# Optimization experiments

Hardware: AMD Instinct MI355X
Metric: run time of the kernel (lower is better)

Reference implementation:

```python
import jax, jax.numpy as jnp
import numpy as np

IN_DIM, OUT_DIM = 64, 64
HIDDEN = [64, 64, 64]
D = IN_DIM * OUT_DIM  # number of independent per-edge small MLPs
B = 256


def setup_inputs() -> dict:
    key = jax.random.key(0)
    ks = jax.random.split(key, 10)

    def kaiming(k, shape, fan_in):
        # kaiming_uniform_ with a=0, nonlinearity='relu': bound = sqrt(6/fan_in)
        bound = np.sqrt(6.0 / fan_in)
        return jax.random.uniform(k, shape, jnp.float32, -bound, bound)

    def bias_init(k, shape, fan_in):
        bound = 1.0 / np.sqrt(fan_in)
        return jax.random.uniform(k, shape, jnp.float32, -bound, bound)

    h0, h1, h2 = HIDDEN
    inp = {
        "x": jax.random.normal(ks[0], (B, IN_DIM), jnp.float32),
        # Input_Linear: weight (out_dim, in_dim, h0); fan_in per torch kaiming on this tensor is in_dim*h0,
        # bias uses reset_parameters(1) -> fan_in=1
        "w0": kaiming(ks[1], (OUT_DIM, IN_DIM, h0), IN_DIM * h0),
        "b0": bias_init(ks[2], (D, h0), 1),
        # Linear(d, o=h1, i=h0): weight (d, h1, h0); kaiming fan_in = h0 (last dim), bias fan_in = i = h0
        "w1": kaiming(ks[3], (D, h1, h0), h0),
        "b1": bias_init(ks[4], (D, h1), h0),
        "w2": kaiming(ks[5], (D, h2, h1), h1),
        "b2": bias_init(ks[6], (D, h2), h1),
        # Output_Linear: weight (out_dim, in_dim*h2), fan_in = in_dim*h2
        "wout": kaiming(ks[7], (OUT_DIM, IN_DIM * h2), IN_DIM * h2),
        "bout": bias_init(ks[8], (OUT_DIM,), IN_DIM * h2),
    }
    return inp


def reference(x, w0, b0, w1, b1, w2, b2, wout, bout):
    Bsz = x.shape[0]
    # Input_Linear: broadcast outer product -> (B, out_dim, in_dim, h0) -> (B, d, h0)
    out = x[:, None, :, None] * w0[None, :, :, :]
    out = out.reshape(Bsz, D, HIDDEN[0]) + b0[None, :, :]
    out = jax.nn.relu(out)
    # Hidden per-edge Linear layers: 'doi,Bdi->Bdo'
    out = jnp.einsum('doi,bdi->bdo', w1, out) + b1[None, :, :]
    out = jax.nn.relu(out)
    out = jnp.einsum('doi,bdi->bdo', w2, out) + b2[None, :, :]
    out = jax.nn.relu(out)
    # Output_Linear: (B, d, h2) -> (B, out_dim, in_dim*h2); 'oi,boi->bo'
    xv = out.reshape(Bsz, OUT_DIM, IN_DIM * HIDDEN[-1])
    return jnp.einsum('oi,boi->bo', wout, xv) + bout[None, :]
```

## Files before the change

### kernel.cpp

```cpp
#include <hip/hip_runtime.h>
#include <hip/hip_bf16.h>


#define D_EDGES 4096

typedef __attribute__((ext_vector_type(4))) float f32x4;
typedef __attribute__((ext_vector_type(8))) short bf16x8;

__device__ __forceinline__ unsigned pk2(float a, float b) {
    __hip_bfloat162 h = __float22bfloat162_rn(float2{a, b});
    return *reinterpret_cast<unsigned*>(&h);
}

union BFr { unsigned u[4]; bf16x8 v; };

__global__ __launch_bounds__(256, 3) void kan_mfma(
    const float* __restrict__ x,
    const float* __restrict__ w0g,
    const float* __restrict__ b0g,
    const float* __restrict__ w1g,
    const float* __restrict__ b1g,
    const float* __restrict__ w2g,
    const float* __restrict__ b2g,
    const float* __restrict__ woutg,
    float* __restrict__ outbuf,
    int atomic_mode)
{
    const int d = blockIdx.x, o = d >> 6, ii = d & 63;
    const int t = threadIdx.x;
    const int lane = t & 63, wv = t >> 6;

    __shared__ __align__(16) unsigned char W1s[64 * 128];
    __shared__ __align__(16) unsigned char W2s[64 * 128];
    __shared__ __align__(16) unsigned char Hs[256 * 128];
    __shared__ __align__(16) float sx[256];
    __shared__ __align__(16) float sw0[64], sb0[64], sb1[64], sb2[64], swo[64];

    {
        const int orow = t >> 2, q = t & 3;
        const unsigned swz  = (unsigned)((orow & 7) << 4);
        const unsigned base = (unsigned)(orow * 128);
        const float* s1 = w1g + (size_t)d * 4096 + orow * 64 + q * 16;
        const float* s2 = w2g + (size_t)d * 4096 + orow * 64 + q * 16;

        float4 a0 = ((const float4*)s1)[0], a1 = ((const float4*)s1)[1];
        float4 a2 = ((const float4*)s1)[2], a3 = ((const float4*)s1)[3];
        uint4 u0 = { pk2(a0.x, a0.y), pk2(a0.z, a0.w), pk2(a1.x, a1.y), pk2(a1.z, a1.w) };
        uint4 u1 = { pk2(a2.x, a2.y), pk2(a2.z, a2.w), pk2(a3.x, a3.y), pk2(a3.z, a3.w) };
        *(uint4*)&W1s[base + ((unsigned)(q * 32)      ^ swz)] = u0;
        *(uint4*)&W1s[base + ((unsigned)(q * 32 + 16) ^ swz)] = u1;

        a0 = ((const float4*)s2)[0]; a1 = ((const float4*)s2)[1];
        a2 = ((const float4*)s2)[2]; a3 = ((const float4*)s2)[3];
        uint4 v0 = { pk2(a0.x, a0.y), pk2(a0.z, a0.w), pk2(a1.x, a1.y), pk2(a1.z, a1.w) };
        uint4 v1 = { pk2(a2.x, a2.y), pk2(a2.z, a2.w), pk2(a3.x, a3.y), pk2(a3.z, a3.w) };
        *(uint4*)&W2s[base + ((unsigned)(q * 32)      ^ swz)] = v0;
        *(uint4*)&W2s[base + ((unsigned)(q * 32 + 16) ^ swz)] = v1;
    }
    sx[t] = x[t * 64 + ii];
    if (t < 64) {
        sw0[t] = w0g[(size_t)d * 64 + t];
        sb0[t] = b0g[(size_t)d * 64 + t];
        sb1[t] = b1g[(size_t)d * 64 + t];
        sb2[t] = b2g[(size_t)d * 64 + t];
        swo[t] = woutg[(size_t)o * 4096 + ii * 64 + t];
    }
    __syncthreads();

    const int arow = lane & 15;
    const int kb   = (lane >> 4) * 16;
    const int g8   = (lane >> 4) * 8;
    const unsigned lswz = (unsigned)((lane & 7) << 4);
    const int mbase = wv * 64;
    const int r0 = (lane >> 4) * 4;
    const f32x4 zero4 = { 0.f, 0.f, 0.f, 0.f };

    bf16x8 wf1[4][2];
#pragma unroll
    for (int nt = 0; nt < 4; ++nt)
#pragma unroll
        for (int ks = 0; ks < 2; ++ks)
            wf1[nt][ks] = *(const bf16x8*)&W1s[(nt * 16 + arow) * 128 +
                            ((unsigned)(ks * 64 + kb) ^ lswz)];

    float4 w0v[2][2], b0v[2][2];
#pragma unroll
    for (int ks = 0; ks < 2; ++ks) {
        const int k0 = ks * 32 + g8;
        w0v[ks][0] = *(const float4*)&sw0[k0];
        w0v[ks][1] = *(const float4*)&sw0[k0 + 4];
        b0v[ks][0] = *(const float4*)&sb0[k0];
        b0v[ks][1] = *(const float4*)&sb0[k0 + 4];
    }

    f32x4 acc[4][4];
#pragma unroll
    for (int i = 0; i < 4; ++i)
#pragma unroll
        for (int j = 0; j < 4; ++j) acc[i][j] = zero4;

#pragma unroll
    for (int mti = 0; mti < 4; ++mti) {
        const float xm = sx[mbase + mti * 16 + arow];
#pragma unroll
        for (int ks = 0; ks < 2; ++ks) {
            float4 wa = w0v[ks][0], wb = w0v[ks][1];
            float4 ba = b0v[ks][0], bb = b0v[ks][1];
            float v0 = fmaxf(fmaf(xm, wa.x, ba.x), 0.f);
            float v1 = fmaxf(fmaf(xm, wa.y, ba.y), 0.f);
            float v2 = fmaxf(fmaf(xm, wa.z, ba.z), 0.f);
            float v3 = fmaxf(fmaf(xm, wa.w, ba.w), 0.f);
            float v4 = fmaxf(fmaf(xm, wb.x, bb.x), 0.f);
            float v5 = fmaxf(fmaf(xm, wb.y, bb.y), 0.f);
            float v6 = fmaxf(fmaf(xm, wb.z, bb.z), 0.f);
            float v7 = fmaxf(fmaf(xm, wb.w, bb.w), 0.f);
            BFr bh;
            bh.u[0] = pk2(v0, v1); bh.u[1] = pk2(v2, v3);
            bh.u[2] = pk2(v4, v5); bh.u[3] = pk2(v6, v7);
#pragma unroll
            for (int nt = 0; nt < 4; ++nt)
                acc[mti][nt] = __builtin_amdgcn_mfma_f32_16x16x32_bf16(
                    wf1[nt][ks], bh.v, acc[mti][nt], 0, 0, 0);
        }
    }

#pragma unroll
    for (int mti = 0; mti < 4; ++mti) {
        const unsigned rb = (unsigned)((mbase + mti * 16 + arow) * 128);
#pragma unroll
        for (int nt = 0; nt < 4; ++nt) {
            float4 bv = *(const float4*)&sb1[nt * 16 + r0];
            float v0 = fmaxf(acc[mti][nt][0] + bv.x, 0.f);
            float v1 = fmaxf(acc[mti][nt][1] + bv.y, 0.f);
            float v2 = fmaxf(acc[mti][nt][2] + bv.z, 0.f);
            float v3 = fmaxf(acc[mti][nt][3] + bv.w, 0.f);
            uint2 hp = { pk2(v0, v1), pk2(v2, v3) };
            *(uint2*)&Hs[rb + ((unsigned)(2 * (nt * 16 + r0)) ^ lswz)] = hp;
        }
    }

    asm volatile("s_waitcnt lgkmcnt(0)" ::: "memory");

    bf16x8 wf2[4][2];
#pragma unroll
    for (int nt = 0; nt < 4; ++nt)
#pragma unroll
        for (int ks = 0; ks < 2; ++ks)
            wf2[nt][ks] = *(const bf16x8*)&W2s[(nt * 16 + arow) * 128 +
                            ((unsigned)(ks * 64 + kb) ^ lswz)];

#pragma unroll
    for (int i = 0; i < 4; ++i)
#pragma unroll
        for (int j = 0; j < 4; ++j) acc[i][j] = zero4;

#pragma unroll
    for (int mti = 0; mti < 4; ++mti) {
        const unsigned rb = (unsigned)((mbase + mti * 16 + arow) * 128);
#pragma unroll
        for (int ks = 0; ks < 2; ++ks) {
            bf16x8 bh = *(const bf16x8*)&Hs[rb + ((unsigned)(ks * 64 + kb) ^ lswz)];
#pragma unroll
            for (int nt = 0; nt < 4; ++nt)
                acc[mti][nt] = __builtin_amdgcn_mfma_f32_16x16x32_bf16(
                    wf2[nt][ks], bh, acc[mti][nt], 0, 0, 0);
        }
    }

#pragma unroll
    for (int mti = 0; mti < 4; ++mti) {
        float p = 0.f;
#pragma unroll
        for (int nt = 0; nt < 4; ++nt) {
            float4 bv = *(const float4*)&sb2[nt * 16 + r0];
            float4 wo = *(const float4*)&swo[nt * 16 + r0];
            p = fmaf(fmaxf(acc[mti][nt][0] + bv.x, 0.f), wo.x, p);
            p = fmaf(fmaxf(acc[mti][nt][1] + bv.y, 0.f), wo.y, p);
            p = fmaf(fmaxf(acc[mti][nt][2] + bv.z, 0.f), wo.z, p);
            p = fmaf(fmaxf(acc[mti][nt][3] + bv.w, 0.f), wo.w, p);
        }
        p += __shfl_xor(p, 16);
        p += __shfl_xor(p, 32);
        const int b = mbase + mti * 16 + arow;
        if (lane < 16) {
            if (atomic_mode) atomicAdd(&outbuf[b * 64 + o], p);
            else             outbuf[(size_t)d * 256 + b] = p;
        }
    }
}

__global__ __launch_bounds__(256) void kan_reduce(
    const float* __restrict__ partial,
    const float* __restrict__ bout,
    float* __restrict__ y)
{
    const int o = blockIdx.x;
    const int b = threadIdx.x;
    float acc = bout[o];
    const float* p = partial + (size_t)o * (64 * 256) + b;
#pragma unroll
    for (int i = 0; i < 64; ++i)
        acc += p[i * 256];
    y[b * 64 + o] = acc;
}

__global__ __launch_bounds__(256) void kan_init_out(const float* __restrict__ bout,
                                                    float* __restrict__ y)
{
    const int idx = blockIdx.x * 256 + threadIdx.x;
    y[idx] = bout[idx & 63];
}

extern "C" void kernel_launch(void* const* d_in, const int* in_sizes, int n_in,
                              void* d_out, int out_size, void* d_ws, size_t ws_size,
                              hipStream_t stream) {
    const float* x    = (const float*)d_in[0];
    const float* w0   = (const float*)d_in[1];
    const float* b0   = (const float*)d_in[2];
    const float* w1   = (const float*)d_in[3];
    const float* b1   = (const float*)d_in[4];
    const float* w2   = (const float*)d_in[5];
    const float* b2   = (const float*)d_in[6];
    const float* wout = (const float*)d_in[7];
    const float* bout = (const float*)d_in[8];
    float* y = (float*)d_out;

    const size_t partial_bytes = (size_t)D_EDGES * 256 * sizeof(float);

    if (ws_size >= partial_bytes) {
        float* partial = (float*)d_ws;
        kan_mfma<<<D_EDGES, 256, 0, stream>>>(x, w0, b0, w1, b1, w2, b2, wout, partial, 0);
        kan_reduce<<<64, 256, 0, stream>>>(partial, bout, y);
    } else {
        kan_init_out<<<64, 256, 0, stream>>>(bout, y);
        kan_mfma<<<D_EDGES, 256, 0, stream>>>(x, w0, b0, w1, b1, w2, b2, wout, y, 1);
    }
}
```

Baseline: 43.25 us.

## Process four edges per block with register-prefetched weights and per-tile hidden staging

New measurement: 105.8 us. 2.45x slower.

```diff
diff --git a/kernel.cpp b/kernel.cpp
--- a/kernel.cpp
+++ b/kernel.cpp
@@ -3,6 +3,7 @@
 
 
 #define D_EDGES 4096
+#define EPB 4
 
 typedef __attribute__((ext_vector_type(4))) float f32x4;
 typedef __attribute__((ext_vector_type(8))) short bf16x8;
@@ -26,165 +27,169 @@
     float* __restrict__ outbuf,
     int atomic_mode)
 {
-    const int d = blockIdx.x, o = d >> 6, ii = d & 63;
     const int t = threadIdx.x;
     const int lane = t & 63, wv = t >> 6;
+    const int d0 = blockIdx.x * EPB;
 
     __shared__ __align__(16) unsigned char W1s[64 * 128];
     __shared__ __align__(16) unsigned char W2s[64 * 128];
-    __shared__ __align__(16) unsigned char Hs[256 * 128];
+    __shared__ __align__(16) unsigned char Hs[4 * 16 * 128];
     __shared__ __align__(16) float sx[256];
     __shared__ __align__(16) float sw0[64], sb0[64], sb1[64], sb2[64], swo[64];
 
-    {
-        const int orow = t >> 2, q = t & 3;
-        const unsigned swz  = (unsigned)((orow & 7) << 4);
-        const unsigned base = (unsigned)(orow * 128);
-        const float* s1 = w1g + (size_t)d * 4096 + orow * 64 + q * 16;
-        const float* s2 = w2g + (size_t)d * 4096 + orow * 64 + q * 16;
-
-        float4 a0 = ((const float4*)s1)[0], a1 = ((const float4*)s1)[1];
-        float4 a2 = ((const float4*)s1)[2], a3 = ((const float4*)s1)[3];
-        uint4 u0 = { pk2(a0.x, a0.y), pk2(a0.z, a0.w), pk2(a1.x, a1.y), pk2(a1.z, a1.w) };
-        uint4 u1 = { pk2(a2.x, a2.y), pk2(a2.z, a2.w), pk2(a3.x, a3.y), pk2(a3.z, a3.w) };
-        *(uint4*)&W1s[base + ((unsigned)(q * 32)      ^ swz)] = u0;
-        *(uint4*)&W1s[base + ((unsigned)(q * 32 + 16) ^ swz)] = u1;
-
-        a0 = ((const float4*)s2)[0]; a1 = ((const float4*)s2)[1];
-        a2 = ((const float4*)s2)[2]; a3 = ((const float4*)s2)[3];
-        uint4 v0 = { pk2(a0.x, a0.y), pk2(a0.z, a0.w), pk2(a1.x, a1.y), pk2(a1.z, a1.w) };
-        uint4 v1 = { pk2(a2.x, a2.y), pk2(a2.z, a2.w), pk2(a3.x, a3.y), pk2(a3.z, a3.w) };
-        *(uint4*)&W2s[base + ((unsigned)(q * 32)      ^ swz)] = v0;
-        *(uint4*)&W2s[base + ((unsigned)(q * 32 + 16) ^ swz)] = v1;
-    }
-    sx[t] = x[t * 64 + ii];
-    if (t < 64) {
-        sw0[t] = w0g[(size_t)d * 64 + t];
-        sb0[t] = b0g[(size_t)d * 64 + t];
-        sb1[t] = b1g[(size_t)d * 64 + t];
-        sb2[t] = b2g[(size_t)d * 64 + t];
-        swo[t] = woutg[(size_t)o * 4096 + ii * 64 + t];
-    }
+    const int orow = t >> 2, q = t & 3;
+    const unsigned wswz  = (unsigned)((orow & 7) << 4);
+    const unsigned wbase = (unsigned)(orow * 128);
+
+    float4 s1r[4], s2r[4];
+    float xv = 0.f, w0r = 0.f, b0r = 0.f, b1r = 0.f, b2r = 0.f, wor = 0.f;
+
+    auto load_edge = [&](int dd) {
+        const float* s1 = w1g + (size_t)dd * 4096 + orow * 64 + q * 16;
+        const float* s2 = w2g + (size_t)dd * 4096 + orow * 64 + q * 16;
+        s1r[0] = ((const float4*)s1)[0]; s1r[1] = ((const float4*)s1)[1];
+        s1r[2] = ((const float4*)s1)[2]; s1r[3] = ((const float4*)s1)[3];
+        s2r[0] = ((const float4*)s2)[0]; s2r[1] = ((const float4*)s2)[1];
+        s2r[2] = ((const float4*)s2)[2]; s2r[3] = ((const float4*)s2)[3];
+        xv = x[t * 64 + (dd & 63)];
+        if (t < 64) {
+            w0r = w0g[(size_t)dd * 64 + t];
+            b0r = b0g[(size_t)dd * 64 + t];
+            b1r = b1g[(size_t)dd * 64 + t];
+            b2r = b2g[(size_t)dd * 64 + t];
+            wor = woutg[(size_t)(dd >> 6) * 4096 + (dd & 63) * 64 + t];
+        }
+    };
+
+    auto store_edge = [&]() {
+        uint4 u0 = { pk2(s1r[0].x, s1r[0].y), pk2(s1r[0].z, s1r[0].w),
+                     pk2(s1r[1].x, s1r[1].y), pk2(s1r[1].z, s1r[1].w) };
+        uint4 u1 = { pk2(s1r[2].x, s1r[2].y), pk2(s1r[2].z, s1r[2].w),
+                     pk2(s1r[3].x, s1r[3].y), pk2(s1r[3].z, s1r[3].w) };
+        *(uint4*)&W1s[wbase + ((unsigned)(q * 32)      ^ wswz)] = u0;
+        *(uint4*)&W1s[wbase + ((unsigned)(q * 32 + 16) ^ wswz)] = u1;
+        uint4 v0 = { pk2(s2r[0].x, s2r[0].y), pk2(s2r[0].z, s2r[0].w),
+                     pk2(s2r[1].x, s2r[1].y), pk2(s2r[1].z, s2r[1].w) };
+        uint4 v1 = { pk2(s2r[2].x, s2r[2].y), pk2(s2r[2].z, s2r[2].w),
+                     pk2(s2r[3].x, s2r[3].y), pk2(s2r[3].z, s2r[3].w) };
+        *(uint4*)&W2s[wbase + ((unsigned)(q * 32)      ^ wswz)] = v0;
+        *(uint4*)&W2s[wbase + ((unsigned)(q * 32 + 16) ^ wswz)] = v1;
+        sx[t] = xv;
+        if (t < 64) {
+            sw0[t] = w0r; sb0[t] = b0r; sb1[t] = b1r; sb2[t] = b2r; swo[t] = wor;
+        }
+    };
+
+    load_edge(d0);
+    store_edge();
     __syncthreads();
 
     const int arow = lane & 15;
     const int kb   = (lane >> 4) * 16;
     const int g8   = (lane >> 4) * 8;
     const unsigned lswz = (unsigned)((lane & 7) << 4);
-    const int mbase = wv * 64;
     const int r0 = (lane >> 4) * 4;
+    const unsigned hbase = (unsigned)(wv * 2048 + arow * 128);
+    const unsigned hswz  = (unsigned)((arow & 7) << 4);
     const f32x4 zero4 = { 0.f, 0.f, 0.f, 0.f };
 
-    bf16x8 wf1[4][2];
-#pragma unroll
-    for (int nt = 0; nt < 4; ++nt)
-#pragma unroll
-        for (int ks = 0; ks < 2; ++ks)
-            wf1[nt][ks] = *(const bf16x8*)&W1s[(nt * 16 + arow) * 128 +
-                            ((unsigned)(ks * 64 + kb) ^ lswz)];
-
-    float4 w0v[2][2], b0v[2][2];
-#pragma unroll
-    for (int ks = 0; ks < 2; ++ks) {
-        const int k0 = ks * 32 + g8;
-        w0v[ks][0] = *(const float4*)&sw0[k0];
-        w0v[ks][1] = *(const float4*)&sw0[k0 + 4];
-        b0v[ks][0] = *(const float4*)&sb0[k0];
-        b0v[ks][1] = *(const float4*)&sb0[k0 + 4];
-    }
-
-    f32x4 acc[4][4];
-#pragma unroll
-    for (int i = 0; i < 4; ++i)
-#pragma unroll
-        for (int j = 0; j < 4; ++j) acc[i][j] = zero4;
-
-#pragma unroll
-    for (int mti = 0; mti < 4; ++mti) {
-        const float xm = sx[mbase + mti * 16 + arow];
+    for (int e = 0; e < EPB; ++e) {
+        const int d = d0 + e;
+        const int o = d >> 6;
+
+        if (e + 1 < EPB) load_edge(d + 1);
+
+        bf16x8 wf1[4][2], wf2[4][2];
+#pragma unroll
+        for (int nt = 0; nt < 4; ++nt)
+#pragma unroll
+            for (int ks = 0; ks < 2; ++ks) {
+                wf1[nt][ks] = *(const bf16x8*)&W1s[(nt * 16 + arow) * 128 +
+                                ((unsigned)(ks * 64 + kb) ^ lswz)];
+                wf2[nt][ks] = *(const bf16x8*)&W2s[(nt * 16 + arow) * 128 +
+                                ((unsigned)(ks * 64 + kb) ^ lswz)];
+            }
+
+        float4 w0v[2][2], b0v[2][2];
 #pragma unroll
         for (int ks = 0; ks < 2; ++ks) {
-            float4 wa = w0v[ks][0], wb = w0v[ks][1];
-            float4 ba = b0v[ks][0], bb = b0v[ks][1];
-            float v0 = fmaxf(fmaf(xm, wa.x, ba.x), 0.f);
-            float v1 = fmaxf(fmaf(xm, wa.y, ba.y), 0.f);
-            float v2 = fmaxf(fmaf(xm, wa.z, ba.z), 0.f);
-            float v3 = fmaxf(fmaf(xm, wa.w, ba.w), 0.f);
-            float v4 = fmaxf(fmaf(xm, wb.x, bb.x), 0.f);
-            float v5 = fmaxf(fmaf(xm, wb.y, bb.y), 0.f);
-            float v6 = fmaxf(fmaf(xm, wb.z, bb.z), 0.f);
-            float v7 = fmaxf(fmaf(xm, wb.w, bb.w), 0.f);
-            BFr bh;
-            bh.u[0] = pk2(v0, v1); bh.u[1] = pk2(v2, v3);
-            bh.u[2] = pk2(v4, v5); bh.u[3] = pk2(v6, v7);
-#pragma unroll
-            for (int nt = 0; nt < 4; ++nt)
-                acc[mti][nt] = __builtin_amdgcn_mfma_f32_16x16x32_bf16(
-                    wf1[nt][ks], bh.v, acc[mti][nt], 0, 0, 0);
-        }
-    }
-
-#pragma unroll
-    for (int mti = 0; mti < 4; ++mti) {
-        const unsigned rb = (unsigned)((mbase + mti * 16 + arow) * 128);
-#pragma unroll
-        for (int nt = 0; nt < 4; ++nt) {
-            float4 bv = *(const float4*)&sb1[nt * 16 + r0];
-            float v0 = fmaxf(acc[mti][nt][0] + bv.x, 0.f);
-            float v1 = fmaxf(acc[mti][nt][1] + bv.y, 0.f);
-            float v2 = fmaxf(acc[mti][nt][2] + bv.z, 0.f);
-            float v3 = fmaxf(acc[mti][nt][3] + bv.w, 0.f);
-            uint2 hp = { pk2(v0, v1), pk2(v2, v3) };
-            *(uint2*)&Hs[rb + ((unsigned)(2 * (nt * 16 + r0)) ^ lswz)] = hp;
-        }
-    }
-
-    asm volatile("s_waitcnt lgkmcnt(0)" ::: "memory");
-
-    bf16x8 wf2[4][2];
-#pragma unroll
-    for (int nt = 0; nt < 4; ++nt)
-#pragma unroll
-        for (int ks = 0; ks < 2; ++ks)
-            wf2[nt][ks] = *(const bf16x8*)&W2s[(nt * 16 + arow) * 128 +
-                            ((unsigned)(ks * 64 + kb) ^ lswz)];
-
-#pragma unroll
-    for (int i = 0; i < 4; ++i)
-#pragma unroll
-        for (int j = 0; j < 4; ++j) acc[i][j] = zero4;
-
-#pragma unroll
-    for (int mti = 0; mti < 4; ++mti) {
-        const unsigned rb = (unsigned)((mbase + mti * 16 + arow) * 128);
-#pragma unroll
-        for (int ks = 0; ks < 2; ++ks) {
-            bf16x8 bh = *(const bf16x8*)&Hs[rb + ((unsigned)(ks * 64 + kb) ^ lswz)];
-#pragma unroll
-            for (int nt = 0; nt < 4; ++nt)
-                acc[mti][nt] = __builtin_amdgcn_mfma_f32_16x16x32_bf16(
-                    wf2[nt][ks], bh, acc[mti][nt], 0, 0, 0);
-        }
-    }
-
-#pragma unroll
-    for (int mti = 0; mti < 4; ++mti) {
-        float p = 0.f;
-#pragma unroll
-        for (int nt = 0; nt < 4; ++nt) {
-            float4 bv = *(const float4*)&sb2[nt * 16 + r0];
-            float4 wo = *(const float4*)&swo[nt * 16 + r0];
-            p = fmaf(fmaxf(acc[mti][nt][0] + bv.x, 0.f), wo.x, p);
-            p = fmaf(fmaxf(acc[mti][nt][1] + bv.y, 0.f), wo.y, p);
-            p = fmaf(fmaxf(acc[mti][nt][2] + bv.z, 0.f), wo.z, p);
-            p = fmaf(fmaxf(acc[mti][nt][3] + bv.w, 0.f), wo.w, p);
-        }
-        p += __shfl_xor(p, 16);
-        p += __shfl_xor(p, 32);
-        const int b = mbase + mti * 16 + arow;
-        if (lane < 16) {
-            if (atomic_mode) atomicAdd(&outbuf[b * 64 + o], p);
-            else             outbuf[(size_t)d * 256 + b] = p;
+            const int k0 = ks * 32 + g8;
+            w0v[ks][0] = *(const float4*)&sw0[k0];
+            w0v[ks][1] = *(const float4*)&sw0[k0 + 4];
+            b0v[ks][0] = *(const float4*)&sb0[k0];
+            b0v[ks][1] = *(const float4*)&sb0[k0 + 4];
+        }
+
+#pragma unroll
+        for (int mti = 0; mti < 4; ++mti) {
+            const float xm = sx[wv * 64 + mti * 16 + arow];
+
+            f32x4 a1[4] = { zero4, zero4, zero4, zero4 };
+#pragma unroll
+            for (int ks = 0; ks < 2; ++ks) {
+                float4 wa = w0v[ks][0], wb = w0v[ks][1];
+                float4 ba = b0v[ks][0], bb = b0v[ks][1];
+                float v0 = fmaxf(fmaf(xm, wa.x, ba.x), 0.f);
+                float v1 = fmaxf(fmaf(xm, wa.y, ba.y), 0.f);
+                float v2 = fmaxf(fmaf(xm, wa.z, ba.z), 0.f);
+                float v3 = fmaxf(fmaf(xm, wa.w, ba.w), 0.f);
+                float v4 = fmaxf(fmaf(xm, wb.x, bb.x), 0.f);
+                float v5 = fmaxf(fmaf(xm, wb.y, bb.y), 0.f);
+                float v6 = fmaxf(fmaf(xm, wb.z, bb.z), 0.f);
+                float v7 = fmaxf(fmaf(xm, wb.w, bb.w), 0.f);
+                BFr bh;
+                bh.u[0] = pk2(v0, v1); bh.u[1] = pk2(v2, v3);
+                bh.u[2] = pk2(v4, v5); bh.u[3] = pk2(v6, v7);
+#pragma unroll
+                for (int nt = 0; nt < 4; ++nt)
+                    a1[nt] = __builtin_amdgcn_mfma_f32_16x16x32_bf16(
+                        wf1[nt][ks], bh.v, a1[nt], 0, 0, 0);
+            }
+
+#pragma unroll
+            for (int nt = 0; nt < 4; ++nt) {
+                float4 bv = *(const float4*)&sb1[nt * 16 + r0];
+                float v0 = fmaxf(a1[nt][0] + bv.x, 0.f);
+                float v1 = fmaxf(a1[nt][1] + bv.y, 0.f);
+                float v2 = fmaxf(a1[nt][2] + bv.z, 0.f);
+                float v3 = fmaxf(a1[nt][3] + bv.w, 0.f);
+                uint2 hp = { pk2(v0, v1), pk2(v2, v3) };
+                *(uint2*)&Hs[hbase + ((unsigned)(2 * (nt * 16 + r0)) ^ hswz)] = hp;
+            }
+
+            f32x4 a2[4] = { zero4, zero4, zero4, zero4 };
+#pragma unroll
+            for (int ks = 0; ks < 2; ++ks) {
+                bf16x8 bh2 = *(const bf16x8*)&Hs[hbase + ((unsigned)(ks * 64 + kb) ^ hswz)];
+#pragma unroll
+                for (int nt = 0; nt < 4; ++nt)
+                    a2[nt] = __builtin_amdgcn_mfma_f32_16x16x32_bf16(
+                        wf2[nt][ks], bh2, a2[nt], 0, 0, 0);
+            }
+
+            float p = 0.f;
+#pragma unroll
+            for (int nt = 0; nt < 4; ++nt) {
+                float4 bv = *(const float4*)&sb2[nt * 16 + r0];
+                float4 wo = *(const float4*)&swo[nt * 16 + r0];
+                p = fmaf(fmaxf(a2[nt][0] + bv.x, 0.f), wo.x, p);
+                p = fmaf(fmaxf(a2[nt][1] + bv.y, 0.f), wo.y, p);
+                p = fmaf(fmaxf(a2[nt][2] + bv.z, 0.f), wo.z, p);
+                p = fmaf(fmaxf(a2[nt][3] + bv.w, 0.f), wo.w, p);
+            }
+            p += __shfl_xor(p, 16);
+            p += __shfl_xor(p, 32);
+            const int b = wv * 64 + mti * 16 + arow;
+            if (lane < 16) {
+                if (atomic_mode) atomicAdd(&outbuf[b * 64 + o], p);
+                else             outbuf[(size_t)d * 256 + b] = p;
+            }
+        }
+
+        if (e + 1 < EPB) {
+            __syncthreads();
+            store_edge();
+            __syncthreads();
         }
     }
 }
@@ -226,13 +231,14 @@
     float* y = (float*)d_out;
 
     const size_t partial_bytes = (size_t)D_EDGES * 256 * sizeof(float);
+    const int nblk = D_EDGES / EPB;
 
     if (ws_size >= partial_bytes) {
         float* partial = (float*)d_ws;
-        kan_mfma<<<D_EDGES, 256, 0, stream>>>(x, w0, b0, w1, b1, w2, b2, wout, partial, 0);
+        kan_mfma<<<nblk, 256, 0, stream>>>(x, w0, b0, w1, b1, w2, b2, wout, partial, 0);
         kan_reduce<<<64, 256, 0, stream>>>(partial, bout, y);
     } else {
         kan_init_out<<<64, 256, 0, stream>>>(bout, y);
-        kan_mfma<<<D_EDGES, 256, 0, stream>>>(x, w0, b0, w1, b1, w2, b2, wout, y, 1);
+        kan_mfma<<<nblk, 256, 0, stream>>>(x, w0, b0, w1, b1, w2, b2, wout, y, 1);
     }
 }
```

## Fuse both hidden layers per 16-row tile to shrink LDS and registers

Applied to the files above, without the earlier changes.

Result: no change. 42.67 us (-1.4%).

```diff
diff --git a/kernel.cpp b/kernel.cpp
--- a/kernel.cpp
+++ b/kernel.cpp
@@ -14,7 +14,7 @@
 
 union BFr { unsigned u[4]; bf16x8 v; };
 
-__global__ __launch_bounds__(256, 3) void kan_mfma(
+__global__ __launch_bounds__(256, 4) void kan_mfma(
     const float* __restrict__ x,
     const float* __restrict__ w0g,
     const float* __restrict__ b0g,
@@ -32,7 +32,7 @@
 
     __shared__ __align__(16) unsigned char W1s[64 * 128];
     __shared__ __align__(16) unsigned char W2s[64 * 128];
-    __shared__ __align__(16) unsigned char Hs[256 * 128];
+    __shared__ __align__(16) unsigned char Hs[4 * 16 * 128];
     __shared__ __align__(16) float sx[256];
     __shared__ __align__(16) float sw0[64], sb0[64], sb1[64], sb2[64], swo[64];
 
@@ -71,8 +71,9 @@
     const int kb   = (lane >> 4) * 16;
     const int g8   = (lane >> 4) * 8;
     const unsigned lswz = (unsigned)((lane & 7) << 4);
-    const int mbase = wv * 64;
     const int r0 = (lane >> 4) * 4;
+    const unsigned hbase = (unsigned)(wv * 2048 + arow * 128);
+    const unsigned hswz  = (unsigned)((arow & 7) << 4);
     const f32x4 zero4 = { 0.f, 0.f, 0.f, 0.f };
 
     bf16x8 wf1[4][2];
@@ -93,15 +94,11 @@
         b0v[ks][1] = *(const float4*)&sb0[k0 + 4];
     }
 
-    f32x4 acc[4][4];
-#pragma unroll
-    for (int i = 0; i < 4; ++i)
-#pragma unroll
-        for (int j = 0; j < 4; ++j) acc[i][j] = zero4;
-
 #pragma unroll
     for (int mti = 0; mti < 4; ++mti) {
-        const float xm = sx[mbase + mti * 16 + arow];
+        const float xm = sx[wv * 64 + mti * 16 + arow];
+
+        f32x4 a1[4] = { zero4, zero4, zero4, zero4 };
 #pragma unroll
         for (int ks = 0; ks < 2; ++ks) {
             float4 wa = w0v[ks][0], wb = w0v[ks][1];
@@ -119,69 +116,47 @@
             bh.u[2] = pk2(v4, v5); bh.u[3] = pk2(v6, v7);
 #pragma unroll
             for (int nt = 0; nt < 4; ++nt)
-                acc[mti][nt] = __builtin_amdgcn_mfma_f32_16x16x32_bf16(
-                    wf1[nt][ks], bh.v, acc[mti][nt], 0, 0, 0);
-        }
-    }
-
-#pragma unroll
-    for (int mti = 0; mti < 4; ++mti) {
-        const unsigned rb = (unsigned)((mbase + mti * 16 + arow) * 128);
+                a1[nt] = __builtin_amdgcn_mfma_f32_16x16x32_bf16(
+                    wf1[nt][ks], bh.v, a1[nt], 0, 0, 0);
+        }
+
 #pragma unroll
         for (int nt = 0; nt < 4; ++nt) {
             float4 bv = *(const float4*)&sb1[nt * 16 + r0];
-            float v0 = fmaxf(acc[mti][nt][0] + bv.x, 0.f);
-            float v1 = fmaxf(acc[mti][nt][1] + bv.y, 0.f);
-            float v2 = fmaxf(acc[mti][nt][2] + bv.z, 0.f);
-            float v3 = fmaxf(acc[mti][nt][3] + bv.w, 0.f);
+            float v0 = fmaxf(a1[nt][0] + bv.x, 0.f);
+            float v1 = fmaxf(a1[nt][1] + bv.y, 0.f);
+            float v2 = fmaxf(a1[nt][2] + bv.z, 0.f);
+            float v3 = fmaxf(a1[nt][3] + bv.w, 0.f);
             uint2 hp = { pk2(v0, v1), pk2(v2, v3) };
-            *(uint2*)&Hs[rb + ((unsigned)(2 * (nt * 16 + r0)) ^ lswz)] = hp;
-        }
-    }
-
-    asm volatile("s_waitcnt lgkmcnt(0)" ::: "memory");
-
-    bf16x8 wf2[4][2];
-#pragma unroll
-    for (int nt = 0; nt < 4; ++nt)
-#pragma unroll
-        for (int ks = 0; ks < 2; ++ks)
-            wf2[nt][ks] = *(const bf16x8*)&W2s[(nt * 16 + arow) * 128 +
-                            ((unsigned)(ks * 64 + kb) ^ lswz)];
-
-#pragma unroll
-    for (int i = 0; i < 4; ++i)
-#pragma unroll
-        for (int j = 0; j < 4; ++j) acc[i][j] = zero4;
-
-#pragma unroll
-    for (int mti = 0; mti < 4; ++mti) {
-        const unsigned rb = (unsigned)((mbase + mti * 16 + arow) * 128);
+            *(uint2*)&Hs[hbase + ((unsigned)(2 * (nt * 16 + r0)) ^ hswz)] = hp;
+        }
+
+        f32x4 a2[4] = { zero4, zero4, zero4, zero4 };
 #pragma unroll
         for (int ks = 0; ks < 2; ++ks) {
-            bf16x8 bh = *(const bf16x8*)&Hs[rb + ((unsigned)(ks * 64 + kb) ^ lswz)];
-#pragma unroll
-            for (int nt = 0; nt < 4; ++nt)
-                acc[mti][nt] = __builtin_amdgcn_mfma_f32_16x16x32_bf16(
-                    wf2[nt][ks], bh, acc[mti][nt], 0, 0, 0);
-        }
-    }
-
-#pragma unroll
-    for (int mti = 0; mti < 4; ++mti) {
+            bf16x8 bh2 = *(const bf16x8*)&Hs[hbase + ((unsigned)(ks * 64 + kb) ^ hswz)];
+#pragma unroll
+            for (int nt = 0; nt < 4; ++nt) {
+                bf16x8 wf2f = *(const bf16x8*)&W2s[(nt * 16 + arow) * 128 +
+                                ((unsigned)(ks * 64 + kb) ^ lswz)];
+                a2[nt] = __builtin_amdgcn_mfma_f32_16x16x32_bf16(
+                    wf2f, bh2, a2[nt], 0, 0, 0);
+            }
+        }
+
         float p = 0.f;
 #pragma unroll
         for (int nt = 0; nt < 4; ++nt) {
             float4 bv = *(const float4*)&sb2[nt * 16 + r0];
             float4 wo = *(const float4*)&swo[nt * 16 + r0];
-            p = fmaf(fmaxf(acc[mti][nt][0] + bv.x, 0.f), wo.x, p);
-            p = fmaf(fmaxf(acc[mti][nt][1] + bv.y, 0.f), wo.y, p);
-            p = fmaf(fmaxf(acc[mti][nt][2] + bv.z, 0.f), wo.z, p);
-            p = fmaf(fmaxf(acc[mti][nt][3] + bv.w, 0.f), wo.w, p);
+            p = fmaf(fmaxf(a2[nt][0] + bv.x, 0.f), wo.x, p);
+            p = fmaf(fmaxf(a2[nt][1] + bv.y, 0.f), wo.y, p);
+            p = fmaf(fmaxf(a2[nt][2] + bv.z, 0.f), wo.z, p);
+            p = fmaf(fmaxf(a2[nt][3] + bv.w, 0.f), wo.w, p);
         }
         p += __shfl_xor(p, 16);
         p += __shfl_xor(p, 32);
-        const int b = mbase + mti * 16 + arow;
+        const int b = wv * 64 + mti * 16 + arow;
         if (lane < 16) {
             if (atomic_mode) atomicAdd(&outbuf[b * 64 + o], p);
             else             outbuf[(size_t)d * 256 + b] = p;
```
